# Kernel tuning notes

Hardware: AMD Instinct MI355X
Metric: run time of the kernel (lower is better)

The kernel has to match this reference:

```python
import jax, jax.numpy as jnp
import numpy as np

N_NODES = 100000
N_EDGES = 1600000
D = 128
L = 3


def setup_inputs() -> dict:
    key = jax.random.key(0)
    k1, k2, k3, k4, k5 = jax.random.split(key, 5)
    x = jax.random.normal(k1, (N_NODES, D), dtype=jnp.float32)
    edge_index = jax.random.randint(k2, (2, N_EDGES), 0, N_NODES, dtype=jnp.int64)
    # Stacked per-layer params (all layers are [D, D] since in==out)
    Wl = jax.random.normal(k3, (L, D, D), dtype=jnp.float32) * 0.05  # lin_l (neighbors), with bias
    bl = jax.random.normal(k4, (L, D), dtype=jnp.float32) * 0.05
    Wr = jax.random.normal(k5, (L, D, D), dtype=jnp.float32) * 0.05  # lin_r (root), no bias
    return {"x": x, "edge_index": edge_index, "Wl": Wl, "bl": bl, "Wr": Wr}


def _sage_conv(x, src, dst, W_l, b_l, W_r):
    # mean aggregation of source features onto target nodes
    msgs = x[src]                                             # [E, D] gather
    agg = jax.ops.segment_sum(msgs, dst, num_segments=N_NODES)  # [N, D] scatter-add
    cnt = jax.ops.segment_sum(jnp.ones((src.shape[0],), x.dtype), dst,
                              num_segments=N_NODES)
    mean = agg / jnp.maximum(cnt, 1.0)[:, None]
    # out = lin_l(mean_neighbors) + lin_r(x)
    return mean @ W_l.T + b_l + x @ W_r.T


def reference(x, edge_index, Wl, bl, Wr):
    src, dst = edge_index[0], edge_index[1]
    for i in range(L):
        x = _sage_conv(x, src, dst, Wl[i], bl[i], Wr[i])
        if i != L - 1:
            x = jax.nn.relu(x)
            # dropout p=0.5 is identity in eval mode
    return jnp.min(x, axis=0)  # [D]
```

## Files before the change

### kernel.cpp

```cpp
#include <hip/hip_runtime.h>
#include <hip/hip_bf16.h>

#define D 128
#define SCAN_C 512
#define BKT 512
#define BKT_SHIFT 9
#define CH 256
#define NBMAX 512
#define MREP 64

typedef __attribute__((ext_vector_type(8))) short bf16x8;
typedef __attribute__((ext_vector_type(4))) float f32x4;

__device__ __forceinline__ float bf16_to_f(unsigned int u) {
    union { unsigned int i; float f; } c; c.i = u << 16; return c.f;
}
__device__ __forceinline__ unsigned short f_to_bf16(float f) {
    union { float f; unsigned int i; } c; c.f = f;
    unsigned int r = c.i + 0x7FFFu + ((c.i >> 16) & 1u);
    return (unsigned short)(r >> 16);
}

__global__ void detect_kernel(const unsigned short* __restrict__ xr,
                              const int* __restrict__ er, int* __restrict__ flag) {
    int plaus = 0;
    for (int i = 0; i < 64; ++i) {
        unsigned short u = xr[2 * i];
        int e = (u >> 7) & 0xFF;
        if (e >= 0x74 && e <= 0x82) plaus++;
    }
    flag[1] = (plaus >= 32) ? 1 : 0;
    int zeros = 0;
    for (int i = 1; i < 128; i += 2) zeros += (er[i] == 0);
    flag[0] = (zeros >= 60) ? 1 : 0;
}

__device__ __forceinline__ int load_idx(const void* p, long long i, int is64) {
    if (is64) return (int)((const long long*)p)[i];
    return ((const int*)p)[i];
}

__global__ void cvt_x_kernel(const void* __restrict__ src, const int* __restrict__ flag,
                             unsigned short* __restrict__ dst, int n) {
    if (flag[1]) return;
    int i = blockIdx.x * blockDim.x + threadIdx.x;
    int stride = gridDim.x * blockDim.x;
    const float* s = (const float*)src;
    for (; i < n; i += stride) dst[i] = f_to_bf16(s[i]);
}

__global__ void cvt_f_kernel(const void* __restrict__ src, const int* __restrict__ flag,
                             float* __restrict__ dst, int n) {
    int is_bf16 = flag[1];
    int i = blockIdx.x * blockDim.x + threadIdx.x;
    int stride = gridDim.x * blockDim.x;
    if (is_bf16) {
        const unsigned short* s = (const unsigned short*)src;
        for (; i < n; i += stride) dst[i] = bf16_to_f(s[i]);
    } else {
        const float* s = (const float*)src;
        for (; i < n; i += stride) dst[i] = s[i];
    }
}

__global__ void packW_kernel(const void* __restrict__ Wl0, const void* __restrict__ Wr0,
                             const int* __restrict__ flag, unsigned short* __restrict__ Wpack,
                             int L) {
    int idx = blockIdx.x * blockDim.x + threadIdx.x;
    if (idx >= L * 8 * 8 * 64) return;
    int lane = idx & 63;
    int ks = (idx >> 6) & 7;
    int nt = (idx >> 9) & 7;
    int layer = idx >> 12;
    int n = nt * 16 + (lane & 15);
    int k0 = ks * 32 + (lane >> 4) * 8;
    int is_bf16 = flag[1];
    unsigned short outv[8];
#pragma unroll
    for (int j = 0; j < 8; ++j) {
        int k = k0 + j;
        size_t off = (size_t)layer * D * D + (size_t)n * D + (k & 127);
        float v;
        if (is_bf16) {
            const unsigned short* W = (const unsigned short*)((k < D) ? Wl0 : Wr0);
            v = bf16_to_f(W[off]);
        } else {
            const float* W = (const float*)((k < D) ? Wl0 : Wr0);
            v = W[off];
        }
        outv[j] = f_to_bf16(v);
    }
    *(uint4*)&Wpack[(size_t)idx * 8] = *(uint4*)outv;
}

__global__ void bucket_hist_kernel(const void* __restrict__ eidx, const int* __restrict__ flag,
                                   int* __restrict__ counts2D, int E, int NB, int EPC) {
    __shared__ int hist[NBMAX];
    int c = blockIdx.x;
    for (int i = threadIdx.x; i < NB; i += blockDim.x) hist[i] = 0;
    __syncthreads();
    int is64 = flag[0];
    int end = min(E, (c + 1) * EPC);
    for (int e = c * EPC + threadIdx.x; e < end; e += blockDim.x) {
        int d = load_idx(eidx, (long long)E + e, is64);
        atomicAdd(&hist[d >> BKT_SHIFT], 1);
    }
    __syncthreads();
    for (int i = threadIdx.x; i < NB; i += blockDim.x)
        counts2D[i * CH + c] = hist[i];
}

__global__ void gscan1_kernel(const int* __restrict__ in, int* __restrict__ blockSums, int n) {
    __shared__ int red[256];
    int base = blockIdx.x * SCAN_C;
    int t = threadIdx.x;
    int s = 0;
    if (base + t < n) s += in[base + t];
    if (base + t + 256 < n) s += in[base + t + 256];
    red[t] = s;
    __syncthreads();
    for (int off = 128; off > 0; off >>= 1) {
        if (t < off) red[t] += red[t + off];
        __syncthreads();
    }
    if (t == 0) blockSums[blockIdx.x] = red[0];
}

__global__ void gscan2_kernel(int* __restrict__ blockSums, int nb) {
    __shared__ int sh[256];
    int t = threadIdx.x;
    int orig = (t < nb) ? blockSums[t] : 0;
    sh[t] = orig;
    __syncthreads();
    for (int off = 1; off < 256; off <<= 1) {
        int v = (t >= off) ? sh[t - off] : 0;
        __syncthreads();
        sh[t] += v;
        __syncthreads();
    }
    if (t < nb) blockSums[t] = sh[t] - orig;
}

__global__ void gscan3_kernel(const int* __restrict__ in, const int* __restrict__ blockBase,
                              int* __restrict__ out, int n) {
    __shared__ int sh[SCAN_C];
    int base = blockIdx.x * SCAN_C;
    int t = threadIdx.x;
    int v0 = (base + t < n) ? in[base + t] : 0;
    int v1 = (base + t + 256 < n) ? in[base + t + 256] : 0;
    sh[t] = v0;
    sh[t + 256] = v1;
    __syncthreads();
    for (int off = 1; off < SCAN_C; off <<= 1) {
        int a = (t >= off) ? sh[t - off] : 0;
        int b = (t + 256 >= off) ? sh[t + 256 - off] : 0;
        __syncthreads();
        sh[t] += a;
        sh[t + 256] += b;
        __syncthreads();
    }
    int bb = blockBase[blockIdx.x];
    if (base + t < n) out[base + t] = bb + sh[t] - v0;
    if (base + t + 256 < n) out[base + t + 256] = bb + sh[t + 256] - v1;
}

__global__ void bucket_scatter_kernel(const void* __restrict__ eidx, const int* __restrict__ flag,
                                      const int* __restrict__ bases2D, unsigned int* __restrict__ ebuf,
                                      int E, int NB, int EPC) {
    __shared__ int cur[NBMAX];
    int c = blockIdx.x;
    for (int i = threadIdx.x; i < NB; i += blockDim.x) cur[i] = bases2D[i * CH + c];
    __syncthreads();
    int is64 = flag[0];
    int end = min(E, (c + 1) * EPC);
    for (int e = c * EPC + threadIdx.x; e < end; e += blockDim.x) {
        int s = load_idx(eidx, e, is64);
        int d = load_idx(eidx, (long long)E + e, is64);
        int b = d >> BKT_SHIFT;
        int pos = atomicAdd(&cur[b], 1);
        ebuf[pos] = ((unsigned)s << BKT_SHIFT) | (unsigned)(d & (BKT - 1));
    }
}

__global__ __launch_bounds__(BKT)
void bucket_csr_kernel(const unsigned int* __restrict__ ebuf, const int* __restrict__ bases2D,
                       int* __restrict__ offsets, int* __restrict__ srcs, int E, int N, int NB) {
    __shared__ int lcnt[BKT];
    __shared__ int sh[BKT];
    __shared__ int lcur[BKT];
    int b = blockIdx.x;
    int t = threadIdx.x;
    int start = bases2D[b * CH];
    int end = (b + 1 < NB) ? bases2D[(b + 1) * CH] : E;
    lcnt[t] = 0;
    __syncthreads();
    for (int e = start + t; e < end; e += BKT)
        atomicAdd(&lcnt[ebuf[e] & (BKT - 1)], 1);
    __syncthreads();
    sh[t] = lcnt[t];
    __syncthreads();
    for (int off = 1; off < BKT; off <<= 1) {
        int v = (t >= off) ? sh[t - off] : 0;
        __syncthreads();
        sh[t] += v;
        __syncthreads();
    }
    int excl = sh[t] - lcnt[t];
    int node = b * BKT + t;
    if (node < N) offsets[node] = start + excl;
    lcur[t] = start + excl;
    __syncthreads();
    for (int e = start + t; e < end; e += BKT) {
        unsigned int p = ebuf[e];
        int pos = atomicAdd(&lcur[p & (BKT - 1)], 1);
        srcs[pos] = (int)(p >> BKT_SHIFT);
    }
    if (b == 0 && t == 0) offsets[N] = E;
}

__global__ void agg_kernel(const unsigned short* __restrict__ xmain,
                           const unsigned short* __restrict__ xalt,
                           const int* __restrict__ flag, const int* __restrict__ offsets,
                           const int* __restrict__ srcs, unsigned short* __restrict__ meanb, int N) {
    const unsigned short* xb = flag[1] ? xalt : xmain;
    int g = blockIdx.x * blockDim.x + threadIdx.x;
    int node = g >> 4;
    int lane = g & 15;
    if (node >= N) return;
    int beg = offsets[node], end = offsets[node + 1];
    float acc[8];
#pragma unroll
    for (int i = 0; i < 8; ++i) acc[i] = 0.f;
    const uint4* xp = (const uint4*)xb;

    int j = beg;
    for (; j + 3 < end; j += 4) {
        int s0 = srcs[j];
        int s1 = srcs[j + 1];
        int s2 = srcs[j + 2];
        int s3 = srcs[j + 3];
        uint4 v0 = xp[(size_t)s0 * 16 + lane];
        uint4 v1 = xp[(size_t)s1 * 16 + lane];
        uint4 v2 = xp[(size_t)s2 * 16 + lane];
        uint4 v3 = xp[(size_t)s3 * 16 + lane];
        acc[0] += bf16_to_f(v0.x & 0xFFFFu); acc[1] += bf16_to_f(v0.x >> 16);
        acc[2] += bf16_to_f(v0.y & 0xFFFFu); acc[3] += bf16_to_f(v0.y >> 16);
        acc[4] += bf16_to_f(v0.z & 0xFFFFu); acc[5] += bf16_to_f(v0.z >> 16);
        acc[6] += bf16_to_f(v0.w & 0xFFFFu); acc[7] += bf16_to_f(v0.w >> 16);
        acc[0] += bf16_to_f(v1.x & 0xFFFFu); acc[1] += bf16_to_f(v1.x >> 16);
        acc[2] += bf16_to_f(v1.y & 0xFFFFu); acc[3] += bf16_to_f(v1.y >> 16);
        acc[4] += bf16_to_f(v1.z & 0xFFFFu); acc[5] += bf16_to_f(v1.z >> 16);
        acc[6] += bf16_to_f(v1.w & 0xFFFFu); acc[7] += bf16_to_f(v1.w >> 16);
        acc[0] += bf16_to_f(v2.x & 0xFFFFu); acc[1] += bf16_to_f(v2.x >> 16);
        acc[2] += bf16_to_f(v2.y & 0xFFFFu); acc[3] += bf16_to_f(v2.y >> 16);
        acc[4] += bf16_to_f(v2.z & 0xFFFFu); acc[5] += bf16_to_f(v2.z >> 16);
        acc[6] += bf16_to_f(v2.w & 0xFFFFu); acc[7] += bf16_to_f(v2.w >> 16);
        acc[0] += bf16_to_f(v3.x & 0xFFFFu); acc[1] += bf16_to_f(v3.x >> 16);
        acc[2] += bf16_to_f(v3.y & 0xFFFFu); acc[3] += bf16_to_f(v3.y >> 16);
        acc[4] += bf16_to_f(v3.z & 0xFFFFu); acc[5] += bf16_to_f(v3.z >> 16);
        acc[6] += bf16_to_f(v3.w & 0xFFFFu); acc[7] += bf16_to_f(v3.w >> 16);
    }
    for (; j < end; ++j) {
        uint4 v = xp[(size_t)srcs[j] * 16 + lane];
        acc[0] += bf16_to_f(v.x & 0xFFFFu); acc[1] += bf16_to_f(v.x >> 16);
        acc[2] += bf16_to_f(v.y & 0xFFFFu); acc[3] += bf16_to_f(v.y >> 16);
        acc[4] += bf16_to_f(v.z & 0xFFFFu); acc[5] += bf16_to_f(v.z >> 16);
        acc[6] += bf16_to_f(v.w & 0xFFFFu); acc[7] += bf16_to_f(v.w >> 16);
    }

    float inv = (end > beg) ? 1.0f / (float)(end - beg) : 0.0f;
    uint4 o;
    o.x = (unsigned)f_to_bf16(acc[0] * inv) | ((unsigned)f_to_bf16(acc[1] * inv) << 16);
    o.y = (unsigned)f_to_bf16(acc[2] * inv) | ((unsigned)f_to_bf16(acc[3] * inv) << 16);
    o.z = (unsigned)f_to_bf16(acc[4] * inv) | ((unsigned)f_to_bf16(acc[5] * inv) << 16);
    o.w = (unsigned)f_to_bf16(acc[6] * inv) | ((unsigned)f_to_bf16(acc[7] * inv) << 16);
    ((uint4*)meanb)[(size_t)node * 16 + lane] = o;
}

__global__ __launch_bounds__(512)
void gemm_mfma_kernel(const unsigned short* __restrict__ meanb,
                      const unsigned short* __restrict__ xmain,
                      const unsigned short* __restrict__ xalt,
                      const int* __restrict__ flag,
                      const unsigned short* __restrict__ Wpack, const float* __restrict__ bl,
                      unsigned short* __restrict__ outb, unsigned int* __restrict__ minbuf,
                      int N, int relu, int do_min) {
    __shared__ unsigned short Wlds[8 * 8 * 64 * 8];
    __shared__ float smin[8][D];
    const unsigned short* xb = flag[1] ? xalt : xmain;

    const int tid = threadIdx.x;
    const int wave = tid >> 6;
    const int lane = tid & 63;
    const int m16 = lane & 15;
    const int quad = lane >> 4;
    const int node0 = blockIdx.x * 128;
    const int arow = node0 + wave * 16 + m16;
    const bool rvalid = arow < N;

    {
        const uint4* wsrc = (const uint4*)Wpack;
        uint4* wdst = (uint4*)Wlds;
#pragma unroll
        for (int i = 0; i < 8; ++i) wdst[tid + i * 512] = wsrc[tid + i * 512];
    }
    __syncthreads();

    f32x4 acc[8];
#pragma unroll
    for (int i = 0; i < 8; ++i) acc[i] = (f32x4)0.0f;

#pragma unroll
    for (int ks = 0; ks < 8; ++ks) {
        uint4 tmp = make_uint4(0u, 0u, 0u, 0u);
        if (rvalid) {
            const unsigned short* base = (ks < 4)
                ? meanb + (size_t)arow * D + ks * 32 + quad * 8
                : xb    + (size_t)arow * D + (ks - 4) * 32 + quad * 8;
            tmp = *(const uint4*)base;
        }
        bf16x8 afrag = *(bf16x8*)&tmp;
#pragma unroll
        for (int nt = 0; nt < 8; ++nt) {
            bf16x8 bfrag = *(const bf16x8*)&Wlds[((nt * 8 + ks) * 64 + lane) * 8];
            acc[nt] = __builtin_amdgcn_mfma_f32_16x16x32_bf16(afrag, bfrag, acc[nt], 0, 0, 0);
        }
    }

    if (do_min) {
#pragma unroll
        for (int nt = 0; nt < 8; ++nt) {
            int n = nt * 16 + m16;
            float b = bl[n];
            float m = 3.402823466e38f;
#pragma unroll
            for (int r = 0; r < 4; ++r) {
                int node = node0 + wave * 16 + quad * 4 + r;
                float v = (node < N) ? (acc[nt][r] + b) : 3.402823466e38f;
                m = fminf(m, v);
            }
            m = fminf(m, __shfl_xor(m, 16, 64));
            m = fminf(m, __shfl_xor(m, 32, 64));
            if (quad == 0) smin[wave][n] = m;
        }
        __syncthreads();
        if (tid < D) {
            float m = smin[0][tid];
#pragma unroll
            for (int w = 1; w < 8; ++w) m = fminf(m, smin[w][tid]);
            unsigned bits = __float_as_uint(m);
            unsigned enc = ((int)bits >= 0) ? (bits ^ 0x80000000u) : ~bits;
            atomicMin(&minbuf[(blockIdx.x & (MREP - 1)) * D + tid], enc);
        }
        return;
    }

    __syncthreads();
    {
        unsigned short (*Ot)[136] = (unsigned short (*)[136])Wlds;
#pragma unroll
        for (int nt = 0; nt < 8; ++nt) {
            int n = nt * 16 + m16;
            float b = bl[n];
#pragma unroll
            for (int r = 0; r < 4; ++r) {
                int m = wave * 16 + quad * 4 + r;
                float v = acc[nt][r] + b;
                if (relu) v = fmaxf(v, 0.f);
                Ot[m][n] = f_to_bf16(v);
            }
        }
        __syncthreads();
        for (int i = tid; i < 128 * 16; i += 512) {
            int row = i >> 4;
            int c = i & 15;
            int n = node0 + row;
            if (n < N) ((uint4*)outb)[(size_t)n * 16 + c] = *(uint4*)&Ot[row][c * 8];
        }
    }
}

__global__ void min_out_kernel(const unsigned int* __restrict__ minbuf,
                               const int* __restrict__ flag, void* __restrict__ out) {
    __shared__ unsigned int sh[4][D];
    int tid = threadIdx.x;
    int q = tid >> 7;
    int c = tid & 127;
    unsigned u = 0xFFFFFFFFu;
    for (int r = q; r < MREP; r += 4) u = min(u, minbuf[r * D + c]);
    sh[q][c] = u;
    __syncthreads();
    if (tid < D) {
        unsigned m = min(min(sh[0][tid], sh[1][tid]), min(sh[2][tid], sh[3][tid]));
        unsigned i = (m & 0x80000000u) ? (m ^ 0x80000000u) : ~m;
        union { unsigned i; float f; } cv; cv.i = i;
        if (flag[1]) ((unsigned short*)out)[tid] = f_to_bf16(cv.f);
        else         ((float*)out)[tid] = cv.f;
    }
}

extern "C" void kernel_launch(void* const* d_in, const int* in_sizes, int n_in,
                              void* d_out, int out_size, void* d_ws, size_t ws_size,
                              hipStream_t stream) {
    const void* x0   = d_in[0];
    const void* eidx = d_in[1];
    const void* Wl0  = d_in[2];
    const void* bl0  = d_in[3];
    const void* Wr0  = d_in[4];

    const int N = in_sizes[0] / D;
    const int E = in_sizes[1] / 2;
    const int L = in_sizes[2] / (D * D);

    char* ws = (char*)d_ws;
    size_t off = 0;
    auto alloc = [&](size_t bytes) -> void* {
        void* p = ws + off;
        off += (bytes + 255) & ~(size_t)255;
        return p;
    };
    unsigned short* xb    = (unsigned short*)alloc((size_t)N * D * 2);
    unsigned short* bufA  = (unsigned short*)alloc((size_t)N * D * 2);
    unsigned short* meanb = (unsigned short*)alloc((size_t)N * D * 2);
    int*   offsets = (int*)alloc((size_t)(N + 1) * sizeof(int));
    int*   srcs    = (int*)alloc((size_t)E * sizeof(int));
    int*   flag    = (int*)alloc(256);
    unsigned short* Wpack = (unsigned short*)alloc((size_t)L * 8 * 8 * 64 * 8 * 2);
    float* blf     = (float*)alloc((size_t)L * D * sizeof(float));
    unsigned int* minbuf = (unsigned int*)alloc((size_t)MREP * D * sizeof(unsigned int));
    (void)ws_size; (void)n_in; (void)out_size;

    const int NB  = (N + BKT - 1) / BKT;
    const int EPC = (E + CH - 1) / CH;
    const int n2  = NB * CH;
    unsigned int* ebuf = (unsigned int*)meanb;
    int* counts2D  = (int*)bufA;
    int* bases2D   = counts2D + n2;
    int* blockSums = bases2D + n2;

    detect_kernel<<<1, 1, 0, stream>>>((const unsigned short*)x0, (const int*)eidx, flag);

    cvt_x_kernel<<<2048, 256, 0, stream>>>(x0, flag, xb, N * D);
    cvt_f_kernel<<<8, 256, 0, stream>>>(bl0, flag, blf, L * D);
    packW_kernel<<<(L * 8 * 8 * 64 + 255) / 256, 256, 0, stream>>>(Wl0, Wr0, flag, Wpack, L);

    hipMemsetAsync(minbuf, 0xFF, (size_t)MREP * D * sizeof(unsigned int), stream);

    bucket_hist_kernel<<<CH, 256, 0, stream>>>(eidx, flag, counts2D, E, NB, EPC);
    const int nb2 = (n2 + SCAN_C - 1) / SCAN_C;
    gscan1_kernel<<<nb2, 256, 0, stream>>>(counts2D, blockSums, n2);
    gscan2_kernel<<<1, 256, 0, stream>>>(blockSums, nb2);
    gscan3_kernel<<<nb2, 256, 0, stream>>>(counts2D, blockSums, bases2D, n2);
    bucket_scatter_kernel<<<CH, 256, 0, stream>>>(eidx, flag, bases2D, ebuf, E, NB, EPC);
    bucket_csr_kernel<<<NB, BKT, 0, stream>>>(ebuf, bases2D, offsets, srcs, E, N, NB);

    const unsigned short* cur     = xb;
    const unsigned short* cur_alt = (const unsigned short*)x0;
    unsigned short* nxt = bufA;
    for (int l = 0; l < L; ++l) {
        int last = (l == L - 1);
        int agg_blocks = (N * 16 + 255) / 256;
        agg_kernel<<<agg_blocks, 256, 0, stream>>>(cur, cur_alt, flag, offsets, srcs, meanb, N);
        gemm_mfma_kernel<<<(N + 127) / 128, 512, 0, stream>>>(
            meanb, cur, cur_alt, flag, Wpack + (size_t)l * 8 * 8 * 64 * 8, blf + (size_t)l * D,
            nxt, minbuf, N, last ? 0 : 1, last);
        cur = nxt; cur_alt = nxt;
        nxt = (nxt == bufA) ? xb : bufA;
    }

    min_out_kernel<<<1, 512, 0, stream>>>(minbuf, flag, (void*)d_out);
}
```

Baseline: 385.3 us.

## Fuse neighbor mean aggregation into the MFMA GEMM kernel via LDS tile

```diff
diff --git a/kernel.cpp b/kernel.cpp
--- a/kernel.cpp
+++ b/kernel.cpp
@@ -218,113 +218,106 @@
     if (b == 0 && t == 0) offsets[N] = E;
 }
 
-__global__ void agg_kernel(const unsigned short* __restrict__ xmain,
-                           const unsigned short* __restrict__ xalt,
-                           const int* __restrict__ flag, const int* __restrict__ offsets,
-                           const int* __restrict__ srcs, unsigned short* __restrict__ meanb, int N) {
+__global__ __launch_bounds__(512, 4)
+void fused_sage_kernel(const unsigned short* __restrict__ xmain,
+                       const unsigned short* __restrict__ xalt,
+                       const int* __restrict__ flag,
+                       const int* __restrict__ offsets,
+                       const int* __restrict__ srcs,
+                       const unsigned short* __restrict__ Wpack,
+                       const float* __restrict__ bl,
+                       unsigned short* __restrict__ outb,
+                       unsigned int* __restrict__ minbuf,
+                       int N, int relu, int do_min) {
+    __shared__ unsigned short Mt[128][136];
+    __shared__ unsigned short Ws[8 * 64 * 8];
+    __shared__ float smin[8][D];
+
     const unsigned short* xb = flag[1] ? xalt : xmain;
-    int g = blockIdx.x * blockDim.x + threadIdx.x;
-    int node = g >> 4;
-    int lane = g & 15;
-    if (node >= N) return;
-    int beg = offsets[node], end = offsets[node + 1];
-    float acc[8];
-#pragma unroll
-    for (int i = 0; i < 8; ++i) acc[i] = 0.f;
     const uint4* xp = (const uint4*)xb;
-
-    int j = beg;
-    for (; j + 3 < end; j += 4) {
-        int s0 = srcs[j];
-        int s1 = srcs[j + 1];
-        int s2 = srcs[j + 2];
-        int s3 = srcs[j + 3];
-        uint4 v0 = xp[(size_t)s0 * 16 + lane];
-        uint4 v1 = xp[(size_t)s1 * 16 + lane];
-        uint4 v2 = xp[(size_t)s2 * 16 + lane];
-        uint4 v3 = xp[(size_t)s3 * 16 + lane];
-        acc[0] += bf16_to_f(v0.x & 0xFFFFu); acc[1] += bf16_to_f(v0.x >> 16);
-        acc[2] += bf16_to_f(v0.y & 0xFFFFu); acc[3] += bf16_to_f(v0.y >> 16);
-        acc[4] += bf16_to_f(v0.z & 0xFFFFu); acc[5] += bf16_to_f(v0.z >> 16);
-        acc[6] += bf16_to_f(v0.w & 0xFFFFu); acc[7] += bf16_to_f(v0.w >> 16);
-        acc[0] += bf16_to_f(v1.x & 0xFFFFu); acc[1] += bf16_to_f(v1.x >> 16);
-        acc[2] += bf16_to_f(v1.y & 0xFFFFu); acc[3] += bf16_to_f(v1.y >> 16);
-        acc[4] += bf16_to_f(v1.z & 0xFFFFu); acc[5] += bf16_to_f(v1.z >> 16);
-        acc[6] += bf16_to_f(v1.w & 0xFFFFu); acc[7] += bf16_to_f(v1.w >> 16);
-        acc[0] += bf16_to_f(v2.x & 0xFFFFu); acc[1] += bf16_to_f(v2.x >> 16);
-        acc[2] += bf16_to_f(v2.y & 0xFFFFu); acc[3] += bf16_to_f(v2.y >> 16);
-        acc[4] += bf16_to_f(v2.z & 0xFFFFu); acc[5] += bf16_to_f(v2.z >> 16);
-        acc[6] += bf16_to_f(v2.w & 0xFFFFu); acc[7] += bf16_to_f(v2.w >> 16);
-        acc[0] += bf16_to_f(v3.x & 0xFFFFu); acc[1] += bf16_to_f(v3.x >> 16);
-        acc[2] += bf16_to_f(v3.y & 0xFFFFu); acc[3] += bf16_to_f(v3.y >> 16);
-        acc[4] += bf16_to_f(v3.z & 0xFFFFu); acc[5] += bf16_to_f(v3.z >> 16);
-        acc[6] += bf16_to_f(v3.w & 0xFFFFu); acc[7] += bf16_to_f(v3.w >> 16);
-    }
-    for (; j < end; ++j) {
-        uint4 v = xp[(size_t)srcs[j] * 16 + lane];
-        acc[0] += bf16_to_f(v.x & 0xFFFFu); acc[1] += bf16_to_f(v.x >> 16);
-        acc[2] += bf16_to_f(v.y & 0xFFFFu); acc[3] += bf16_to_f(v.y >> 16);
-        acc[4] += bf16_to_f(v.z & 0xFFFFu); acc[5] += bf16_to_f(v.z >> 16);
-        acc[6] += bf16_to_f(v.w & 0xFFFFu); acc[7] += bf16_to_f(v.w >> 16);
-    }
-
-    float inv = (end > beg) ? 1.0f / (float)(end - beg) : 0.0f;
-    uint4 o;
-    o.x = (unsigned)f_to_bf16(acc[0] * inv) | ((unsigned)f_to_bf16(acc[1] * inv) << 16);
-    o.y = (unsigned)f_to_bf16(acc[2] * inv) | ((unsigned)f_to_bf16(acc[3] * inv) << 16);
-    o.z = (unsigned)f_to_bf16(acc[4] * inv) | ((unsigned)f_to_bf16(acc[5] * inv) << 16);
-    o.w = (unsigned)f_to_bf16(acc[6] * inv) | ((unsigned)f_to_bf16(acc[7] * inv) << 16);
-    ((uint4*)meanb)[(size_t)node * 16 + lane] = o;
-}
-
-__global__ __launch_bounds__(512)
-void gemm_mfma_kernel(const unsigned short* __restrict__ meanb,
-                      const unsigned short* __restrict__ xmain,
-                      const unsigned short* __restrict__ xalt,
-                      const int* __restrict__ flag,
-                      const unsigned short* __restrict__ Wpack, const float* __restrict__ bl,
-                      unsigned short* __restrict__ outb, unsigned int* __restrict__ minbuf,
-                      int N, int relu, int do_min) {
-    __shared__ unsigned short Wlds[8 * 8 * 64 * 8];
-    __shared__ float smin[8][D];
-    const unsigned short* xb = flag[1] ? xalt : xmain;
-
     const int tid = threadIdx.x;
     const int wave = tid >> 6;
     const int lane = tid & 63;
+    const int node0 = blockIdx.x * 128;
+
+    {
+        const int g  = tid >> 4;
+        const int gl = tid & 15;
+        const int gw = g & 3;
+        const int r0 = wave * 16 + gw * 4;
+        for (int i = 0; i < 4; ++i) {
+            const int row = r0 + i;
+            const int node = node0 + row;
+            float acc[8];
+#pragma unroll
+            for (int q = 0; q < 8; ++q) acc[q] = 0.f;
+            int beg = 0, end = 0;
+            if (node < N) { beg = offsets[node]; end = offsets[node + 1]; }
+            for (int j = beg; j < end; j += 16) {
+                const int nrem = end - j;
+                int myS = 0;
+                if (gl < nrem) myS = __builtin_nontemporal_load(&srcs[j + gl]);
+                if (nrem >= 16) {
+#pragma unroll
+                    for (int e = 0; e < 16; ++e) {
+                        int s = __shfl(myS, (gw << 4) + e, 64);
+                        uint4 v = xp[(size_t)s * 16 + gl];
+                        acc[0] += bf16_to_f(v.x & 0xFFFFu); acc[1] += bf16_to_f(v.x >> 16);
+                        acc[2] += bf16_to_f(v.y & 0xFFFFu); acc[3] += bf16_to_f(v.y >> 16);
+                        acc[4] += bf16_to_f(v.z & 0xFFFFu); acc[5] += bf16_to_f(v.z >> 16);
+                        acc[6] += bf16_to_f(v.w & 0xFFFFu); acc[7] += bf16_to_f(v.w >> 16);
+                    }
+                } else {
+                    for (int e = 0; e < nrem; ++e) {
+                        int s = __shfl(myS, (gw << 4) + e, 64);
+                        uint4 v = xp[(size_t)s * 16 + gl];
+                        acc[0] += bf16_to_f(v.x & 0xFFFFu); acc[1] += bf16_to_f(v.x >> 16);
+                        acc[2] += bf16_to_f(v.y & 0xFFFFu); acc[3] += bf16_to_f(v.y >> 16);
+                        acc[4] += bf16_to_f(v.z & 0xFFFFu); acc[5] += bf16_to_f(v.z >> 16);
+                        acc[6] += bf16_to_f(v.w & 0xFFFFu); acc[7] += bf16_to_f(v.w >> 16);
+                    }
+                }
+            }
+            float inv = (end > beg) ? 1.0f / (float)(end - beg) : 0.f;
+            uint4 o;
+            o.x = (unsigned)f_to_bf16(acc[0] * inv) | ((unsigned)f_to_bf16(acc[1] * inv) << 16);
+            o.y = (unsigned)f_to_bf16(acc[2] * inv) | ((unsigned)f_to_bf16(acc[3] * inv) << 16);
+            o.z = (unsigned)f_to_bf16(acc[4] * inv) | ((unsigned)f_to_bf16(acc[5] * inv) << 16);
+            o.w = (unsigned)f_to_bf16(acc[6] * inv) | ((unsigned)f_to_bf16(acc[7] * inv) << 16);
+            *(uint4*)&Mt[row][(gl ^ (row & 15)) << 3] = o;
+        }
+    }
+    __syncthreads();
+
     const int m16 = lane & 15;
     const int quad = lane >> 4;
-    const int node0 = blockIdx.x * 128;
     const int arow = node0 + wave * 16 + m16;
     const bool rvalid = arow < N;
-
-    {
-        const uint4* wsrc = (const uint4*)Wpack;
-        uint4* wdst = (uint4*)Wlds;
-#pragma unroll
-        for (int i = 0; i < 8; ++i) wdst[tid + i * 512] = wsrc[tid + i * 512];
-    }
-    __syncthreads();
-
-    f32x4 acc[8];
-#pragma unroll
-    for (int i = 0; i < 8; ++i) acc[i] = (f32x4)0.0f;
-
-#pragma unroll
+    const uint4* wsrc = (const uint4*)Wpack;
+    uint4* Wsv = (uint4*)Ws;
+
+    f32x4 acc2[8];
+#pragma unroll
+    for (int i = 0; i < 8; ++i) acc2[i] = (f32x4)0.0f;
+
     for (int ks = 0; ks < 8; ++ks) {
-        uint4 tmp = make_uint4(0u, 0u, 0u, 0u);
-        if (rvalid) {
-            const unsigned short* base = (ks < 4)
-                ? meanb + (size_t)arow * D + ks * 32 + quad * 8
-                : xb    + (size_t)arow * D + (ks - 4) * 32 + quad * 8;
-            tmp = *(const uint4*)base;
-        }
-        bf16x8 afrag = *(bf16x8*)&tmp;
+        uint4 wv = wsrc[(wave * 8 + ks) * 64 + lane];
+        bf16x8 afrag;
+        if (ks < 4) {
+            afrag = *(bf16x8*)&Mt[wave * 16 + m16][((((ks << 2) + quad)) ^ m16) << 3];
+        } else {
+            uint4 tmp = make_uint4(0u, 0u, 0u, 0u);
+            if (rvalid) tmp = *(const uint4*)(xb + (size_t)arow * D + (ks - 4) * 32 + quad * 8);
+            afrag = *(bf16x8*)&tmp;
+        }
+        Wsv[tid] = wv;
+        __syncthreads();
 #pragma unroll
         for (int nt = 0; nt < 8; ++nt) {
-            bf16x8 bfrag = *(const bf16x8*)&Wlds[((nt * 8 + ks) * 64 + lane) * 8];
-            acc[nt] = __builtin_amdgcn_mfma_f32_16x16x32_bf16(afrag, bfrag, acc[nt], 0, 0, 0);
-        }
+            bf16x8 bfrag = *(const bf16x8*)&Ws[(nt * 64 + lane) << 3];
+            acc2[nt] = __builtin_amdgcn_mfma_f32_16x16x32_bf16(afrag, bfrag, acc2[nt], 0, 0, 0);
+        }
+        __syncthreads();
     }
 
     if (do_min) {
@@ -336,7 +329,7 @@
 #pragma unroll
             for (int r = 0; r < 4; ++r) {
                 int node = node0 + wave * 16 + quad * 4 + r;
-                float v = (node < N) ? (acc[nt][r] + b) : 3.402823466e38f;
+                float v = (node < N) ? (acc2[nt][r] + b) : 3.402823466e38f;
                 m = fminf(m, v);
             }
             m = fminf(m, __shfl_xor(m, 16, 64));
@@ -355,9 +348,8 @@
         return;
     }
 
-    __syncthreads();
     {
-        unsigned short (*Ot)[136] = (unsigned short (*)[136])Wlds;
+        unsigned short (*Ot)[136] = Mt;
 #pragma unroll
         for (int nt = 0; nt < 8; ++nt) {
             int n = nt * 16 + m16;
@@ -365,7 +357,7 @@
 #pragma unroll
             for (int r = 0; r < 4; ++r) {
                 int m = wave * 16 + quad * 4 + r;
-                float v = acc[nt][r] + b;
+                float v = acc2[nt][r] + b;
                 if (relu) v = fmaxf(v, 0.f);
                 Ot[m][n] = f_to_bf16(v);
             }
@@ -421,7 +413,7 @@
     };
     unsigned short* xb    = (unsigned short*)alloc((size_t)N * D * 2);
     unsigned short* bufA  = (unsigned short*)alloc((size_t)N * D * 2);
-    unsigned short* meanb = (unsigned short*)alloc((size_t)N * D * 2);
+    unsigned short* scratch = (unsigned short*)alloc((size_t)N * D * 2);
     int*   offsets = (int*)alloc((size_t)(N + 1) * sizeof(int));
     int*   srcs    = (int*)alloc((size_t)E * sizeof(int));
     int*   flag    = (int*)alloc(256);
@@ -433,7 +425,7 @@
     const int NB  = (N + BKT - 1) / BKT;
     const int EPC = (E + CH - 1) / CH;
     const int n2  = NB * CH;
-    unsigned int* ebuf = (unsigned int*)meanb;
+    unsigned int* ebuf = (unsigned int*)scratch;
     int* counts2D  = (int*)bufA;
     int* bases2D   = counts2D + n2;
     int* blockSums = bases2D + n2;
@@ -459,10 +451,9 @@
     unsigned short* nxt = bufA;
     for (int l = 0; l < L; ++l) {
         int last = (l == L - 1);
-        int agg_blocks = (N * 16 + 255) / 256;
-        agg_kernel<<<agg_blocks, 256, 0, stream>>>(cur, cur_alt, flag, offsets, srcs, meanb, N);
-        gemm_mfma_kernel<<<(N + 127) / 128, 512, 0, stream>>>(
-            meanb, cur, cur_alt, flag, Wpack + (size_t)l * 8 * 8 * 64 * 8, blf + (size_t)l * D,
+        fused_sage_kernel<<<(N + 127) / 128, 512, 0, stream>>>(
+            cur, cur_alt, flag, offsets, srcs,
+            Wpack + (size_t)l * 8 * 8 * 64 * 8, blf + (size_t)l * D,
             nxt, minbuf, N, last ? 0 : 1, last);
         cur = nxt; cur_alt = nxt;
         nxt = (nxt == bufA) ? xb : bufA;
```

Measured after the change: 492.5 us. +27.8%, slower.
